# Performance work log

Hardware: AMD Instinct MI355X
Metric: run time of the kernel (lower is better)

Reference implementation:

```python
import jax, jax.numpy as jnp
import numpy as np

D_MODEL = 256
NHEAD = 8
D_K = D_MODEL // NHEAD
IM_SIZE = 8
SCALE = float(IM_SIZE ** 2)  # sqrt(im_size**4)


def setup_inputs() -> dict:
    key = jax.random.key(0)
    ks = jax.random.split(key, 9)
    B, P, S = 8, 256, 8
    s = 1.0 / np.sqrt(D_MODEL)
    return {
        "x": jax.random.normal(ks[0], (B, P, S, S, D_MODEL), jnp.float32),
        "Wq": jax.random.normal(ks[1], (D_MODEL, D_MODEL), jnp.float32) * s,
        "bq": jax.random.normal(ks[2], (D_MODEL,), jnp.float32) * s,
        "Wk": jax.random.normal(ks[3], (D_MODEL, D_MODEL), jnp.float32) * s,
        "bk": jax.random.normal(ks[4], (D_MODEL,), jnp.float32) * s,
        "Wv": jax.random.normal(ks[5], (D_MODEL, D_MODEL), jnp.float32) * s,
        "bv": jax.random.normal(ks[6], (D_MODEL,), jnp.float32) * s,
        "Wo": jax.random.normal(ks[7], (D_MODEL, D_MODEL), jnp.float32) * s,
        "bo": jax.random.normal(ks[8], (D_MODEL,), jnp.float32) * s,
    }


def _split_heads(t):
    # torch: view(..., d_k, nhead).permute(0,5,1,2,3,4) -> [b, n, p, x, y, d_k]
    b, p, sx, sy, _ = t.shape
    t = t.reshape(b, p, sx, sy, D_K, NHEAD)
    return jnp.transpose(t, (0, 5, 1, 2, 3, 4))


def reference(x, Wq, bq, Wk, bk, Wv, bv, Wo, bo):
    Q = _split_heads(x @ Wq.T + bq)
    K = _split_heads(x @ Wk.T + bk)
    V = _split_heads(x @ Wv.T + bv)
    # scores over flattened (x, y, d_k) dims
    scores = jnp.einsum('bnpxyd,bnqxyd->bnpq', Q, K) / SCALE
    attn = jax.nn.softmax(scores, axis=-1)
    out = jnp.einsum('bnpq,bnqxyd->bnpxyd', attn, V)
    # permute to [b, p, x, y, d_k, n] then merge (d_k, n) -> d_model
    out = jnp.transpose(out, (0, 2, 3, 4, 5, 1))
    b, p, sx, sy, _, _ = out.shape
    out = out.reshape(b, p, sx, sy, NHEAD * D_K)
    return out @ Wo.T + bo
```

## Files before the change

### kernel.cpp

```cpp
#include <hip/hip_runtime.h>
#include <hip/hip_bf16.h>


typedef __bf16 bf16;
typedef __attribute__((ext_vector_type(8))) __bf16 bf16x8;
typedef __attribute__((ext_vector_type(4))) float floatx4;
typedef __attribute__((ext_vector_type(8))) unsigned short ushort8;

#define CDIM 2048

static __device__ __forceinline__ floatx4 mfma16(bf16x8 a, bf16x8 b, floatx4 c) {
  return __builtin_amdgcn_mfma_f32_16x16x32_bf16(a, b, c, 0, 0, 0);
}

static __device__ __forceinline__ void gload_lds16(const void* g, void* l) {
  __builtin_amdgcn_global_load_lds((const __attribute__((address_space(1))) void*)g,
                                   (__attribute__((address_space(3))) void*)l, 16, 0, 0);
}

__global__ __launch_bounds__(256) void k0_prep(
    const float* __restrict__ Wq, const float* __restrict__ bq,
    const float* __restrict__ Wk, const float* __restrict__ bk,
    const float* __restrict__ Wv, const float* __restrict__ bv,
    const float* __restrict__ Wo,
    bf16* __restrict__ Wp, bf16* __restrict__ Wk3, float* __restrict__ biasp)
{
  const int bid = blockIdx.x, tid = threadIdx.x;
  int g = (bid & 31) * 256 + tid;
  int lane = g & 63, rowblk = (g >> 6) & 15, kk = g >> 10;
  int h = lane >> 4, cl = lane & 15;
  int d0 = kk * 32 + 8 * h;
  if (bid < 32) {
    int ip = rowblk * 16 + cl;
    int isrc = ((ip & 31) << 3) | (ip >> 5);
#pragma unroll
    for (int mat = 0; mat < 3; mat++) {
      const float* W = (mat == 0) ? Wq : (mat == 1) ? Wk : Wv;
      bf16x8 v;
#pragma unroll
      for (int j = 0; j < 8; j++) v[j] = (bf16)W[isrc * 256 + d0 + j];
      *reinterpret_cast<bf16x8*>(Wp + ((size_t)mat * 8192 + g) * 8) = v;
    }
    if (bid == 0 && tid < 256) {
      int bs = ((tid & 31) << 3) | (tid >> 5);
      biasp[tid] = bq[bs]; biasp[256 + tid] = bk[bs]; biasp[512 + tid] = bv[bs];
    }
  } else {
    int j = rowblk * 16 + cl;
    bf16x8 v;
#pragma unroll
    for (int jj = 0; jj < 8; jj++) {
      int c = d0 + jj;
      v[jj] = (bf16)Wo[j * 256 + (((c & 31) << 3) | (c >> 5))];
    }
    *reinterpret_cast<bf16x8*>(Wk3 + (size_t)g * 8) = v;
  }
}

__global__ __launch_bounds__(512, 6) void k1_qkv(
    const float* __restrict__ x, const bf16* __restrict__ Wp,
    const float* __restrict__ biasp,
    bf16* __restrict__ Qs, bf16* __restrict__ Ks, bf16* __restrict__ Vt)
{
  __shared__ bf16 xsb[64 * 256];
  const int g = blockIdx.x;
  const int a = g / 24;
  const int rem = g - a * 24;
  const int mat = rem >> 3;
  const int t0 = (a * 8 + (rem & 7)) * 64;
  const int tid = threadIdx.x;
  const int lane = tid & 63;
  const int w = tid >> 6;
  const int h = lane >> 4, cl = lane & 15;
  const int c7 = cl & 7;

  const bf16* Wm = Wp + (size_t)mat * 65536;

#pragma unroll
  for (int k = 0; k < 4; ++k) {
    int G = k * 512 + tid;
    int row = G >> 5;
    const float* sp = x + (size_t)(t0 + row) * 256 + (G & 31) * 8;
    floatx4 f0 = *reinterpret_cast<const floatx4*>(sp);
    floatx4 f1 = *reinterpret_cast<const floatx4*>(sp + 4);
    bf16x8 v;
#pragma unroll
    for (int j = 0; j < 4; j++) { v[j] = (bf16)f0[j]; v[4 + j] = (bf16)f1[j]; }
    int Gp = (G & ~7) | ((G ^ row) & 7);
    *reinterpret_cast<bf16x8*>(&xsb[Gp * 8]) = v;
  }
  __syncthreads();

  floatx4 acc[4][2];
#pragma unroll
  for (int i = 0; i < 4; i++)
#pragma unroll
    for (int j = 0; j < 2; j++) acc[i][j] = (floatx4)0.0f;

#pragma unroll 2
  for (int kk = 0; kk < 8; ++kk) {
    bf16x8 av[4];
#pragma unroll
    for (int mt = 0; mt < 4; mt++) {
      int rr = mt * 16 + cl;
      int G = rr * 32 + kk * 4 + h;
      int Gp = (G & ~7) | ((G ^ c7) & 7);
      av[mt] = *reinterpret_cast<const bf16x8*>(&xsb[Gp * 8]);
    }
    bf16x8 b0 = *reinterpret_cast<const bf16x8*>(
        Wm + ((size_t)(kk * 16 + w * 2 + 0) * 64 + lane) * 8);
    bf16x8 b1 = *reinterpret_cast<const bf16x8*>(
        Wm + ((size_t)(kk * 16 + w * 2 + 1) * 64 + lane) * 8);
#pragma unroll
    for (int mt = 0; mt < 4; mt++) acc[mt][0] = mfma16(av[mt], b0, acc[mt][0]);
#pragma unroll
    for (int mt = 0; mt < 4; mt++) acc[mt][1] = mfma16(av[mt], b1, acc[mt][1]);
  }

  const int b = t0 >> 14;
  const int p = (t0 >> 6) & 255;
  if (mat < 2) {
    bf16* ob = ((mat == 0) ? Qs : Ks) + ((size_t)(b * 8 + w) * 256 + p) * 2048;
#pragma unroll
    for (int nt = 0; nt < 2; nt++) {
      const int ip = w * 32 + nt * 16 + cl;
      const float bb = biasp[mat * 256 + ip];
      const int dk = nt * 16 + cl;
#pragma unroll
      for (int mt = 0; mt < 4; mt++)
#pragma unroll
        for (int r = 0; r < 4; r++) {
          int sxy = mt * 16 + 4 * h + r;
          ob[sxy * 32 + dk] = (bf16)(acc[mt][nt][r] + bb);
        }
    }
  } else {
#pragma unroll
    for (int nt = 0; nt < 2; nt++) {
      const int ip = w * 32 + nt * 16 + cl;
      const float bb = biasp[512 + ip];
#pragma unroll
      for (int mt = 0; mt < 4; mt++)
#pragma unroll
        for (int r = 0; r < 4; r++) {
          int t = t0 + mt * 16 + 4 * h + r;
          Vt[(size_t)t * 256 + ip] = (bf16)(acc[mt][nt][r] + bb);
        }
    }
  }
}

__global__ __launch_bounds__(1024, 4) void k2a_scores(
    const bf16* __restrict__ Qs, const bf16* __restrict__ Ks,
    bf16* __restrict__ attn)
{
  __shared__ bf16 Qch[2][128 * 64];
  __shared__ bf16 Kch[2][256 * 64];
  __shared__ float redmax[4][4][32];
  __shared__ float redsum[4][4][32];

  const int bx = blockIdx.x;
  const int bn = bx & 63;
  const int p0 = (bx >> 6) * 128;
  const int tid = threadIdx.x;
  const int lane = tid & 63;
  const int w = tid >> 6;
  const int wr = w >> 2, wc = w & 3;
  const int h = lane >> 4, cl = lane & 15;

  const bf16* Qb = Qs + (size_t)bn * 524288 + (size_t)p0 * 2048;
  const bf16* Kb = Ks + (size_t)bn * 524288;

  const int Lq = w * 64 + lane;
  const int rq = Lq >> 3, sq = (Lq & 7) ^ (rq & 7);
  const size_t qsrc = (size_t)rq * 2048 + sq * 8;
  int rk[2]; size_t ksrc[2];
#pragma unroll
  for (int i = 0; i < 2; ++i) {
    int L = i * 1024 + w * 64 + lane;
    rk[i] = L >> 3;
    int s = (L & 7) ^ (rk[i] & 7);
    ksrc[i] = (size_t)rk[i] * 2048 + s * 8;
  }

#define K2A_STAGE(bufi, c)                                                  \
  {                                                                         \
    gload_lds16(Qb + qsrc + (c) * 64, &Qch[bufi][(w * 64) * 8]);            \
    gload_lds16(Kb + ksrc[0] + (c) * 64, &Kch[bufi][(w * 64) * 8]);         \
    gload_lds16(Kb + ksrc[1] + (c) * 64, &Kch[bufi][(1024 + w * 64) * 8]);  \
  }

  floatx4 acc[2][4];
#pragma unroll
  for (int i = 0; i < 2; i++)
#pragma unroll
    for (int j = 0; j < 4; j++) acc[i][j] = (floatx4)0.0f;

  K2A_STAGE(0, 0);
  __syncthreads();
  int buf = 0;
  for (int c = 0; c < 32; ++c) {
    if (c + 1 < 32) K2A_STAGE(buf ^ 1, c + 1);
#pragma unroll
    for (int kk = 0; kk < 2; ++kk) {
      bf16x8 av[2], bv[4];
#pragma unroll
      for (int mt = 0; mt < 2; mt++) {
        int row = wr * 32 + mt * 16 + cl;
        int gg = kk * 4 + h;
        av[mt] = *reinterpret_cast<const bf16x8*>(
            &Qch[buf][(row * 8 + (gg ^ (row & 7))) * 8]);
      }
#pragma unroll
      for (int nt = 0; nt < 4; nt++) {
        int row = wc * 64 + nt * 16 + cl;
        int gg = kk * 4 + h;
        bv[nt] = *reinterpret_cast<const bf16x8*>(
            &Kch[buf][(row * 8 + (gg ^ (row & 7))) * 8]);
      }
#pragma unroll
      for (int nt = 0; nt < 4; nt++)
#pragma unroll
        for (int mt = 0; mt < 2; mt++)
          acc[mt][nt] = mfma16(av[mt], bv[nt], acc[mt][nt]);
    }
    __syncthreads();
    buf ^= 1;
  }

  float pm[2][4];
#pragma unroll
  for (int mt = 0; mt < 2; mt++)
#pragma unroll
    for (int r = 0; r < 4; r++)
      pm[mt][r] = fmaxf(fmaxf(acc[mt][0][r], acc[mt][1][r]),
                        fmaxf(acc[mt][2][r], acc[mt][3][r]));
#pragma unroll
  for (int off = 1; off < 16; off <<= 1)
#pragma unroll
    for (int mt = 0; mt < 2; mt++)
#pragma unroll
      for (int r = 0; r < 4; r++)
        pm[mt][r] = fmaxf(pm[mt][r], __shfl_xor(pm[mt][r], off, 64));
  if (cl == 0) {
#pragma unroll
    for (int mt = 0; mt < 2; mt++)
#pragma unroll
      for (int r = 0; r < 4; r++) redmax[wr][wc][mt * 16 + 4 * h + r] = pm[mt][r];
  }
  __syncthreads();

  float gm[2][4], ps[2][4];
#pragma unroll
  for (int mt = 0; mt < 2; mt++)
#pragma unroll
    for (int r = 0; r < 4; r++) {
      int row = mt * 16 + 4 * h + r;
      gm[mt][r] = fmaxf(fmaxf(redmax[wr][0][row], redmax[wr][1][row]),
                        fmaxf(redmax[wr][2][row], redmax[wr][3][row]));
      ps[mt][r] = 0.0f;
    }
  const float KS = 1.44269504088896340736f / 64.0f;
#pragma unroll
  for (int mt = 0; mt < 2; mt++)
#pragma unroll
    for (int nt = 0; nt < 4; nt++)
#pragma unroll
      for (int r = 0; r < 4; r++) {
        float e = exp2f((acc[mt][nt][r] - gm[mt][r]) * KS);
        acc[mt][nt][r] = e;
        ps[mt][r] += e;
      }
#pragma unroll
  for (int off = 1; off < 16; off <<= 1)
#pragma unroll
    for (int mt = 0; mt < 2; mt++)
#pragma unroll
      for (int r = 0; r < 4; r++) ps[mt][r] += __shfl_xor(ps[mt][r], off, 64);
  if (cl == 0) {
#pragma unroll
    for (int mt = 0; mt < 2; mt++)
#pragma unroll
      for (int r = 0; r < 4; r++) redsum[wr][wc][mt * 16 + 4 * h + r] = ps[mt][r];
  }
  __syncthreads();

#pragma unroll
  for (int mt = 0; mt < 2; mt++)
#pragma unroll
    for (int r = 0; r < 4; r++) {
      int row = mt * 16 + 4 * h + r;
      float gs = (redsum[wr][0][row] + redsum[wr][1][row])
               + (redsum[wr][2][row] + redsum[wr][3][row]);
      ps[mt][r] = 1.0f / gs;
    }
#pragma unroll
  for (int nt = 0; nt < 4; nt++) {
    int q = wc * 64 + nt * 16 + cl;
#pragma unroll
    for (int mt = 0; mt < 2; mt++)
#pragma unroll
      for (int r = 0; r < 4; r++) {
        int row = p0 + wr * 32 + mt * 16 + 4 * h + r;
        attn[(size_t)bn * 65536 + row * 256 + q] = (bf16)(acc[mt][nt][r] * ps[mt][r]);
      }
  }
#undef K2A_STAGE
}

__global__ __launch_bounds__(256) void k2t_transpose(
    const bf16* __restrict__ Vtok, bf16* __restrict__ Vq)
{
  const int bx = blockIdx.x;
  const int bn = bx & 63;
  const int r2 = bx >> 6;
  const int q0 = (r2 & 3) * 64;
  const int c0 = (r2 >> 2) * 64;
  const int b = bn >> 3, n = bn & 7;
  __shared__ unsigned short tile[64][65];
  const unsigned short* src = (const unsigned short*)Vtok;
  unsigned short* dst = (unsigned short*)Vq + (size_t)bn * 524288;
  {
    const int q = threadIdx.x >> 3;
    const int cj = (threadIdx.x & 7) * 8;
    const int c = c0 + cj;
    const int sxy = c >> 5, dk0 = c & 31;
#pragma unroll
    for (int it = 0; it < 2; ++it) {
      int qq = q + it * 32;
      size_t sa = (size_t)((b * 256 + q0 + qq) * 64 + sxy) * 256 + n * 32 + dk0;
      ushort8 s = *reinterpret_cast<const ushort8*>(src + sa);
#pragma unroll
      for (int j = 0; j < 8; j++) tile[qq][cj + j] = s[j];
    }
  }
  __syncthreads();
  {
    const int crow = threadIdx.x >> 2;
    const int qj = (threadIdx.x & 3) * 8;
#pragma unroll
    for (int it = 0; it < 2; ++it) {
      int qq = qj + it * 32;
      ushort8 sv;
#pragma unroll
      for (int j = 0; j < 8; j++) sv[j] = tile[qq + j][crow];
      *reinterpret_cast<ushort8*>(dst + (size_t)(c0 + crow) * 256 + q0 + qq) = sv;
    }
  }
}

__global__ __launch_bounds__(512, 6) void k2b_pv(
    const bf16* __restrict__ attn, const bf16* __restrict__ Vq,
    bf16* __restrict__ yhat)
{
  __shared__ bf16 As[64 * 256];
  const int bx = blockIdx.x;
  const int bn = bx & 63;
  const int r2 = bx >> 6;
  const int p0 = (r2 & 3) * 64;
  const int c0 = (r2 >> 2) * 256;
  const int b = bn >> 3, n = bn & 7;
  const int tid = threadIdx.x;
  const int lane = tid & 63;
  const int w = tid >> 6;
  const int h = lane >> 4, cl = lane & 15;
  const int c7 = cl & 7;

  const bf16* Ab = attn + (size_t)bn * 65536 + (size_t)p0 * 256;
  const bf16* Vb = Vq + (size_t)bn * 524288;

#pragma unroll
  for (int i = 0; i < 4; ++i) {
    int L = (i * 8 + w) * 64 + lane;
    int S = (L & ~7) | ((L ^ (L >> 5)) & 7);
    gload_lds16(Ab + (size_t)S * 8, &As[(size_t)(i * 8 + w) * 64 * 8]);
  }
  __syncthreads();

  floatx4 acc[4][2];
#pragma unroll
  for (int i = 0; i < 4; i++)
#pragma unroll
    for (int j = 0; j < 2; j++) acc[i][j] = (floatx4)0.0f;

#pragma unroll 2
  for (int kk = 0; kk < 8; ++kk) {
    bf16x8 av[4];
#pragma unroll
    for (int mt = 0; mt < 4; mt++) {
      int rr = mt * 16 + cl;
      int G = rr * 32 + kk * 4 + h;
      int Gp = (G & ~7) | ((G ^ c7) & 7);
      av[mt] = *reinterpret_cast<const bf16x8*>(&As[Gp * 8]);
    }
    bf16x8 b0 = *reinterpret_cast<const bf16x8*>(
        Vb + (size_t)(c0 + w * 32 + cl) * 256 + kk * 32 + 8 * h);
    bf16x8 b1 = *reinterpret_cast<const bf16x8*>(
        Vb + (size_t)(c0 + w * 32 + 16 + cl) * 256 + kk * 32 + 8 * h);
#pragma unroll
    for (int mt = 0; mt < 4; mt++) acc[mt][0] = mfma16(av[mt], b0, acc[mt][0]);
#pragma unroll
    for (int mt = 0; mt < 4; mt++) acc[mt][1] = mfma16(av[mt], b1, acc[mt][1]);
  }

#pragma unroll
  for (int nt = 0; nt < 2; nt++) {
    const int cg = c0 + w * 32 + nt * 16 + cl;
    const int dk = cg & 31, sxy = cg >> 5;
#pragma unroll
    for (int mt = 0; mt < 4; mt++)
#pragma unroll
      for (int r = 0; r < 4; r++) {
        int p = p0 + mt * 16 + 4 * h + r;
        size_t t = (size_t)((b * 256 + p) * 64) + sxy;
        yhat[t * 256 + n * 32 + dk] = (bf16)acc[mt][nt][r];
      }
  }
}

__global__ __launch_bounds__(512, 6) void k3_out(
    const bf16* __restrict__ yhat, const bf16* __restrict__ Wk3,
    const float* __restrict__ bo, float* __restrict__ outp)
{
  __shared__ bf16 As[64 * 256];
  const int t0 = blockIdx.x * 64;
  const int tid = threadIdx.x;
  const int lane = tid & 63;
  const int w = tid >> 6;
  const int h = lane >> 4, cl = lane & 15;
  const int c7 = cl & 7;

  const bf16* Ab = yhat + (size_t)t0 * 256;

#pragma unroll
  for (int i = 0; i < 4; ++i) {
    int L = (i * 8 + w) * 64 + lane;
    int S = (L & ~7) | ((L ^ (L >> 5)) & 7);
    gload_lds16(Ab + (size_t)S * 8, &As[(size_t)(i * 8 + w) * 64 * 8]);
  }
  __syncthreads();

  floatx4 acc[4][2];
#pragma unroll
  for (int i = 0; i < 4; i++)
#pragma unroll
    for (int j = 0; j < 2; j++) acc[i][j] = (floatx4)0.0f;

#pragma unroll 2
  for (int kk = 0; kk < 8; ++kk) {
    bf16x8 av[4];
#pragma unroll
    for (int mt = 0; mt < 4; mt++) {
      int rr = mt * 16 + cl;
      int G = rr * 32 + kk * 4 + h;
      int Gp = (G & ~7) | ((G ^ c7) & 7);
      av[mt] = *reinterpret_cast<const bf16x8*>(&As[Gp * 8]);
    }
    bf16x8 b0 = *reinterpret_cast<const bf16x8*>(
        Wk3 + ((size_t)(kk * 16 + w * 2 + 0) * 64 + lane) * 8);
    bf16x8 b1 = *reinterpret_cast<const bf16x8*>(
        Wk3 + ((size_t)(kk * 16 + w * 2 + 1) * 64 + lane) * 8);
#pragma unroll
    for (int mt = 0; mt < 4; mt++) acc[mt][0] = mfma16(av[mt], b0, acc[mt][0]);
#pragma unroll
    for (int mt = 0; mt < 4; mt++) acc[mt][1] = mfma16(av[mt], b1, acc[mt][1]);
  }

#pragma unroll
  for (int nt = 0; nt < 2; nt++) {
    const int j = w * 32 + nt * 16 + cl;
    const float bb = bo[j];
#pragma unroll
    for (int mt = 0; mt < 4; mt++)
#pragma unroll
      for (int r = 0; r < 4; r++)
        outp[(size_t)(t0 + mt * 16 + 4 * h + r) * 256 + j] = acc[mt][nt][r] + bb;
  }
}

extern "C" void kernel_launch(void* const* d_in, const int* in_sizes, int n_in,
                              void* d_out, int out_size, void* d_ws, size_t ws_size,
                              hipStream_t stream) {
  const float* x  = (const float*)d_in[0];
  const float* Wq = (const float*)d_in[1];
  const float* bq = (const float*)d_in[2];
  const float* Wk = (const float*)d_in[3];
  const float* bk = (const float*)d_in[4];
  const float* Wv = (const float*)d_in[5];
  const float* bv = (const float*)d_in[6];
  const float* Wo = (const float*)d_in[7];
  const float* bo = (const float*)d_in[8];
  float* outp = (float*)d_out;

  char* ws = (char*)d_ws;
  const size_t SZ_QKV = 67108864;
  size_t off = 0;
  bf16* Qs   = (bf16*)(ws + off); off += SZ_QKV;
  bf16* Ks   = (bf16*)(ws + off); off += SZ_QKV;
  bf16* Vtok = (bf16*)(ws + off); off += SZ_QKV;
  bf16* attn = (bf16*)(ws + off); off += 8388608;
  bf16* Wp   = (bf16*)(ws + off); off += 393216;
  bf16* Wk3  = (bf16*)(ws + off); off += 131072;
  float* biasp = (float*)(ws + off); off += 3072;
  if (ws_size < off) return;

  bf16* yhat = Qs;
  bf16* Vq   = Ks;

  k0_prep<<<64, 256, 0, stream>>>(Wq, bq, Wk, bk, Wv, bv, Wo, Wp, Wk3, biasp);
  k1_qkv<<<6144, 512, 0, stream>>>(x, Wp, biasp, Qs, Ks, Vtok);
  k2a_scores<<<128, 1024, 0, stream>>>(Qs, Ks, attn);
  k2t_transpose<<<8192, 256, 0, stream>>>(Vtok, Vq);
  k2b_pv<<<2048, 512, 0, stream>>>(attn, Vq, yhat);
  k3_out<<<2048, 512, 0, stream>>>(yhat, Wk3, bo, outp);
}
```

Measured before the change: 313.9 us.

## Make QKV projection persistent with double-buffered register prefetch of x tiles

The QKV projection kernel now launches a quarter as many blocks. Each block processes four tiles in sequence, loading the next x tile into registers while it computes the current one from a double-buffered LDS array. The aim is to hide global-load latency behind MFMA work and cut block launch overhead. In exchange it doubles LDS per block, lowers the occupancy hint from 6 to 4, and adds register pressure from the prefetch buffers.

```diff
diff --git a/kernel.cpp b/kernel.cpp
--- a/kernel.cpp
+++ b/kernel.cpp
@@ -57,97 +57,132 @@
   }
 }
 
-__global__ __launch_bounds__(512, 6) void k1_qkv(
+__global__ __launch_bounds__(512, 4) void k1_qkv(
     const float* __restrict__ x, const bf16* __restrict__ Wp,
     const float* __restrict__ biasp,
     bf16* __restrict__ Qs, bf16* __restrict__ Ks, bf16* __restrict__ Vt)
 {
-  __shared__ bf16 xsb[64 * 256];
-  const int g = blockIdx.x;
-  const int a = g / 24;
-  const int rem = g - a * 24;
-  const int mat = rem >> 3;
-  const int t0 = (a * 8 + (rem & 7)) * 64;
+  __shared__ bf16 buf[2][64 * 256];
+  const int bx = blockIdx.x;
   const int tid = threadIdx.x;
   const int lane = tid & 63;
   const int w = tid >> 6;
   const int h = lane >> 4, cl = lane & 15;
   const int c7 = cl & 7;
 
-  const bf16* Wm = Wp + (size_t)mat * 65536;
-
-#pragma unroll
-  for (int k = 0; k < 4; ++k) {
-    int G = k * 512 + tid;
-    int row = G >> 5;
-    const float* sp = x + (size_t)(t0 + row) * 256 + (G & 31) * 8;
-    floatx4 f0 = *reinterpret_cast<const floatx4*>(sp);
-    floatx4 f1 = *reinterpret_cast<const floatx4*>(sp + 4);
-    bf16x8 v;
-#pragma unroll
-    for (int j = 0; j < 4; j++) { v[j] = (bf16)f0[j]; v[4 + j] = (bf16)f1[j]; }
-    int Gp = (G & ~7) | ((G ^ row) & 7);
-    *reinterpret_cast<bf16x8*>(&xsb[Gp * 8]) = v;
-  }
-  __syncthreads();
-
-  floatx4 acc[4][2];
-#pragma unroll
-  for (int i = 0; i < 4; i++)
-#pragma unroll
-    for (int j = 0; j < 2; j++) acc[i][j] = (floatx4)0.0f;
-
-#pragma unroll 2
-  for (int kk = 0; kk < 8; ++kk) {
-    bf16x8 av[4];
-#pragma unroll
-    for (int mt = 0; mt < 4; mt++) {
-      int rr = mt * 16 + cl;
-      int G = rr * 32 + kk * 4 + h;
-      int Gp = (G & ~7) | ((G ^ c7) & 7);
-      av[mt] = *reinterpret_cast<const bf16x8*>(&xsb[Gp * 8]);
-    }
-    bf16x8 b0 = *reinterpret_cast<const bf16x8*>(
-        Wm + ((size_t)(kk * 16 + w * 2 + 0) * 64 + lane) * 8);
-    bf16x8 b1 = *reinterpret_cast<const bf16x8*>(
-        Wm + ((size_t)(kk * 16 + w * 2 + 1) * 64 + lane) * 8);
-#pragma unroll
-    for (int mt = 0; mt < 4; mt++) acc[mt][0] = mfma16(av[mt], b0, acc[mt][0]);
-#pragma unroll
-    for (int mt = 0; mt < 4; mt++) acc[mt][1] = mfma16(av[mt], b1, acc[mt][1]);
-  }
-
-  const int b = t0 >> 14;
-  const int p = (t0 >> 6) & 255;
-  if (mat < 2) {
-    bf16* ob = ((mat == 0) ? Qs : Ks) + ((size_t)(b * 8 + w) * 256 + p) * 2048;
-#pragma unroll
-    for (int nt = 0; nt < 2; nt++) {
-      const int ip = w * 32 + nt * 16 + cl;
-      const float bb = biasp[mat * 256 + ip];
-      const int dk = nt * 16 + cl;
-#pragma unroll
-      for (int mt = 0; mt < 4; mt++)
-#pragma unroll
-        for (int r = 0; r < 4; r++) {
-          int sxy = mt * 16 + 4 * h + r;
-          ob[sxy * 32 + dk] = (bf16)(acc[mt][nt][r] + bb);
-        }
-    }
-  } else {
-#pragma unroll
-    for (int nt = 0; nt < 2; nt++) {
-      const int ip = w * 32 + nt * 16 + cl;
-      const float bb = biasp[512 + ip];
-#pragma unroll
-      for (int mt = 0; mt < 4; mt++)
-#pragma unroll
-        for (int r = 0; r < 4; r++) {
-          int t = t0 + mt * 16 + 4 * h + r;
-          Vt[(size_t)t * 256 + ip] = (bf16)(acc[mt][nt][r] + bb);
-        }
-    }
-  }
+  floatx4 sreg[8];
+
+#define K1_LOAD(VB)                                                          \
+  {                                                                          \
+    int a_ = (VB) / 24;                                                      \
+    int t0_ = (a_ * 8 + ((VB) & 7)) * 64;                                    \
+    _Pragma("unroll")                                                        \
+    for (int k = 0; k < 4; ++k) {                                            \
+      int G = k * 512 + tid;                                                 \
+      int row = G >> 5;                                                      \
+      const float* sp = x + (size_t)(t0_ + row) * 256 + (G & 31) * 8;        \
+      sreg[2 * k]     = *reinterpret_cast<const floatx4*>(sp);               \
+      sreg[2 * k + 1] = *reinterpret_cast<const floatx4*>(sp + 4);           \
+    }                                                                        \
+  }
+
+#define K1_CVTWRITE(BUFI)                                                    \
+  {                                                                          \
+    _Pragma("unroll")                                                        \
+    for (int k = 0; k < 4; ++k) {                                            \
+      int G = k * 512 + tid;                                                 \
+      int row = G >> 5;                                                      \
+      bf16x8 v;                                                              \
+      _Pragma("unroll")                                                      \
+      for (int j = 0; j < 4; j++) {                                          \
+        v[j] = (bf16)sreg[2 * k][j];                                         \
+        v[4 + j] = (bf16)sreg[2 * k + 1][j];                                 \
+      }                                                                      \
+      int Gp = (G & ~7) | ((G ^ row) & 7);                                   \
+      *reinterpret_cast<bf16x8*>(&buf[BUFI][Gp * 8]) = v;                    \
+    }                                                                        \
+  }
+
+#define K1_COMPUTE(VB, BUFI)                                                 \
+  {                                                                          \
+    int a_ = (VB) / 24;                                                      \
+    int rem_ = (VB) - a_ * 24;                                               \
+    int mat_ = rem_ >> 3;                                                    \
+    int t0_ = (a_ * 8 + (rem_ & 7)) * 64;                                    \
+    const bf16* Wm = Wp + (size_t)mat_ * 65536;                              \
+    floatx4 acc[4][2];                                                       \
+    _Pragma("unroll")                                                        \
+    for (int i = 0; i < 4; i++)                                              \
+      _Pragma("unroll")                                                      \
+      for (int j = 0; j < 2; j++) acc[i][j] = (floatx4)0.0f;                 \
+    _Pragma("unroll 2")                                                      \
+    for (int kk = 0; kk < 8; ++kk) {                                         \
+      bf16x8 av[4];                                                          \
+      _Pragma("unroll")                                                      \
+      for (int mt = 0; mt < 4; mt++) {                                       \
+        int rr = mt * 16 + cl;                                               \
+        int G = rr * 32 + kk * 4 + h;                                        \
+        int Gp = (G & ~7) | ((G ^ c7) & 7);                                  \
+        av[mt] = *reinterpret_cast<const bf16x8*>(&buf[BUFI][Gp * 8]);       \
+      }                                                                      \
+      bf16x8 b0 = *reinterpret_cast<const bf16x8*>(                          \
+          Wm + ((size_t)(kk * 16 + w * 2 + 0) * 64 + lane) * 8);             \
+      bf16x8 b1 = *reinterpret_cast<const bf16x8*>(                          \
+          Wm + ((size_t)(kk * 16 + w * 2 + 1) * 64 + lane) * 8);             \
+      _Pragma("unroll")                                                      \
+      for (int mt = 0; mt < 4; mt++) acc[mt][0] = mfma16(av[mt], b0, acc[mt][0]); \
+      _Pragma("unroll")                                                      \
+      for (int mt = 0; mt < 4; mt++) acc[mt][1] = mfma16(av[mt], b1, acc[mt][1]); \
+    }                                                                        \
+    int b_ = t0_ >> 14;                                                      \
+    int p_ = (t0_ >> 6) & 255;                                               \
+    if (mat_ < 2) {                                                          \
+      bf16* ob = ((mat_ == 0) ? Qs : Ks) + ((size_t)(b_ * 8 + w) * 256 + p_) * 2048; \
+      _Pragma("unroll")                                                      \
+      for (int nt = 0; nt < 2; nt++) {                                       \
+        const int ip = w * 32 + nt * 16 + cl;                                \
+        const float bb = biasp[mat_ * 256 + ip];                             \
+        const int dk = nt * 16 + cl;                                         \
+        _Pragma("unroll")                                                    \
+        for (int mt = 0; mt < 4; mt++)                                       \
+          _Pragma("unroll")                                                  \
+          for (int r = 0; r < 4; r++) {                                      \
+            int sxy = mt * 16 + 4 * h + r;                                   \
+            ob[sxy * 32 + dk] = (bf16)(acc[mt][nt][r] + bb);                 \
+          }                                                                  \
+      }                                                                      \
+    } else {                                                                 \
+      _Pragma("unroll")                                                      \
+      for (int nt = 0; nt < 2; nt++) {                                       \
+        const int ip = w * 32 + nt * 16 + cl;                                \
+        const float bb = biasp[512 + ip];                                    \
+        _Pragma("unroll")                                                    \
+        for (int mt = 0; mt < 4; mt++)                                       \
+          _Pragma("unroll")                                                  \
+          for (int r = 0; r < 4; r++) {                                      \
+            int t = t0_ + mt * 16 + 4 * h + r;                               \
+            Vt[(size_t)t * 256 + ip] = (bf16)(acc[mt][nt][r] + bb);          \
+          }                                                                  \
+      }                                                                      \
+    }                                                                        \
+  }
+
+  K1_LOAD(bx);
+  K1_CVTWRITE(0);
+  __syncthreads();
+#pragma unroll
+  for (int u = 1; u < 4; ++u) {
+    K1_LOAD(bx + u * 1536);
+    K1_COMPUTE(bx + (u - 1) * 1536, (u - 1) & 1);
+    __syncthreads();
+    K1_CVTWRITE(u & 1);
+    __syncthreads();
+  }
+  K1_COMPUTE(bx + 3 * 1536, 1);
+
+#undef K1_LOAD
+#undef K1_CVTWRITE
+#undef K1_COMPUTE
 }
 
 __global__ __launch_bounds__(1024, 4) void k2a_scores(
@@ -508,7 +543,7 @@
   bf16* Vq   = Ks;
 
   k0_prep<<<64, 256, 0, stream>>>(Wq, bq, Wk, bk, Wv, bv, Wo, Wp, Wk3, biasp);
-  k1_qkv<<<6144, 512, 0, stream>>>(x, Wp, biasp, Qs, Ks, Vtok);
+  k1_qkv<<<1536, 512, 0, stream>>>(x, Wp, biasp, Qs, Ks, Vtok);
   k2a_scores<<<128, 1024, 0, stream>>>(Qs, Ks, attn);
   k2t_transpose<<<8192, 256, 0, stream>>>(Vtok, Vq);
   k2b_pv<<<2048, 512, 0, stream>>>(attn, Vq, yhat);
```

Measured after the change: 311.9 us. Within noise of the previous version (-0.6%).
